# Performance work log

Hardware: AMD Instinct MI355X
Metric: run time of the kernel (lower is better)

The kernel has to match this reference:

```python
import jax, jax.numpy as jnp
import numpy as np


def setup_inputs() -> dict:
    key = jax.random.key(0)
    k1, k2, k3 = jax.random.split(key, 3)
    Na, Nb, D, K = 1024, 1024, 512, 256
    a = jax.random.normal(k1, (Na, D), dtype=jnp.float32)
    b = jax.random.normal(k2, (Nb, D), dtype=jnp.float32)
    feats = jax.random.normal(k3, (K, D), dtype=jnp.float32)
    return {"a": a, "b": b, "feats": feats}


def reference(a, b, feats):
    # 'ignorematch' mode of the Difference module.
    # Project both sets onto the feature bank: [Na,K] and [Nb,K]
    a_fk = jnp.matmul(a, feats.T)          # [Na, K]
    b_fk = jnp.matmul(b, feats.T)          # [Nb, K]
    a_e = a_fk[:, None, :]                 # [Na, 1, K]
    b_e = b_fk[None, :, :]                 # [1, Nb, K]
    # features present in a (>0) but absent in b (<=0)
    mask = ((a_e > 0) & (b_e <= 0)).astype(a_fk.dtype)  # [Na, Nb, K]
    result = jnp.sum(a_e * mask, axis=2)   # [Na, Nb]
    return result
```

## Files before the change

kernel.cpp:

```cpp
#include <hip/hip_runtime.h>
#include <hip/hip_bf16.h>


typedef short bf16x8 __attribute__((ext_vector_type(8)));
typedef float f32x4  __attribute__((ext_vector_type(4)));

__device__ inline void split2s(float x, short& h, short& m) {
    __hip_bfloat16 hb = __float2bfloat16(x);
    float r1 = x - __bfloat162float(hb);
    __hip_bfloat16 mb = __float2bfloat16(r1);
    h = *(short*)&hb; m = *(short*)&mb;
}

__device__ inline void split3s(float x, short& h, short& m, short& l) {
    __hip_bfloat16 hb = __float2bfloat16(x);
    float r1 = x - __bfloat162float(hb);
    __hip_bfloat16 mb = __float2bfloat16(r1);
    float r2 = r1 - __bfloat162float(mb);
    __hip_bfloat16 lb = __float2bfloat16(r2);
    h = *(short*)&hb; m = *(short*)&mb; l = *(short*)&lb;
}

__device__ inline void grid_barrier(unsigned* cnt, unsigned* flag, int nblk) {
    __syncthreads();
    if (threadIdx.x == 0) {
        __threadfence();
        unsigned prev = __hip_atomic_fetch_add(cnt, 1u, __ATOMIC_RELAXED,
                                               __HIP_MEMORY_SCOPE_AGENT);
        if (prev == (unsigned)(nblk - 1)) {
            __hip_atomic_store(flag, 1u, __ATOMIC_RELAXED, __HIP_MEMORY_SCOPE_AGENT);
        } else {
            while (__hip_atomic_load(flag, __ATOMIC_RELAXED,
                                     __HIP_MEMORY_SCOPE_AGENT) == 0u)
                __builtin_amdgcn_s_sleep(32);
        }
        __threadfence();
    }
    __syncthreads();
}

__global__ __launch_bounds__(256) void fused_kernel(
    const float* __restrict__ a, const float* __restrict__ b, const float* __restrict__ f,
    unsigned* __restrict__ bar,
    __hip_bfloat16* __restrict__ pbf, __hip_bfloat16* __restrict__ mbf,
    float* __restrict__ out)
{
    const int tid  = threadIdx.x;
    const int w    = tid >> 6;
    const int lane = tid & 63;
    const int l15  = lane & 15;
    const int q    = lane >> 4;

    {
        const int jb = blockIdx.x;
        const int m0 = (jb >> 3) * 32;
        const int n0 = (jb & 7) * 32;
        const int wi = w >> 1, wj = w & 1;

        const float* ap = a + (size_t)(m0 + wi * 16 + l15) * 512;
        const float* bp = b + (size_t)(m0 + wi * 16 + l15) * 512;
        const float* fp = f + (size_t)(n0 + wj * 16 + l15) * 512;

        f32x4 accA = {0.f, 0.f, 0.f, 0.f};
        f32x4 accB = {0.f, 0.f, 0.f, 0.f};

        #pragma unroll 2
        for (int k0 = 0; k0 < 512; k0 += 32) {
            const int ko = k0 + q * 8;
            float4 a0 = *(const float4*)(ap + ko);
            float4 a1 = *(const float4*)(ap + ko + 4);
            float4 b0 = *(const float4*)(bp + ko);
            float4 b1 = *(const float4*)(bp + ko + 4);
            float4 f0 = *(const float4*)(fp + ko);
            float4 f1 = *(const float4*)(fp + ko + 4);

            bf16x8 ah, am, bh, bm, bl, fh, fm, fl;
            const float av_[8] = {a0.x, a0.y, a0.z, a0.w, a1.x, a1.y, a1.z, a1.w};
            const float bv_[8] = {b0.x, b0.y, b0.z, b0.w, b1.x, b1.y, b1.z, b1.w};
            const float fv_[8] = {f0.x, f0.y, f0.z, f0.w, f1.x, f1.y, f1.z, f1.w};
            #pragma unroll
            for (int i = 0; i < 8; i++) {
                short h, m, l;
                split2s(av_[i], h, m);        ah[i] = h; am[i] = m;
                split3s(bv_[i], h, m, l);     bh[i] = h; bm[i] = m; bl[i] = l;
                split3s(fv_[i], h, m, l);     fh[i] = h; fm[i] = m; fl[i] = l;
            }

            accA = __builtin_amdgcn_mfma_f32_16x16x32_bf16(ah, fh, accA, 0, 0, 0);
            accB = __builtin_amdgcn_mfma_f32_16x16x32_bf16(bh, fh, accB, 0, 0, 0);
            accA = __builtin_amdgcn_mfma_f32_16x16x32_bf16(ah, fm, accA, 0, 0, 0);
            accB = __builtin_amdgcn_mfma_f32_16x16x32_bf16(bh, fm, accB, 0, 0, 0);
            accA = __builtin_amdgcn_mfma_f32_16x16x32_bf16(am, fh, accA, 0, 0, 0);
            accB = __builtin_amdgcn_mfma_f32_16x16x32_bf16(bm, fh, accB, 0, 0, 0);
            accB = __builtin_amdgcn_mfma_f32_16x16x32_bf16(bh, fl, accB, 0, 0, 0);
            accB = __builtin_amdgcn_mfma_f32_16x16x32_bf16(bl, fh, accB, 0, 0, 0);
            accB = __builtin_amdgcn_mfma_f32_16x16x32_bf16(bm, fm, accB, 0, 0, 0);
        }

        const int orow = m0 + wi * 16 + q * 4;
        const int ocol = n0 + wj * 16 + l15;
        #pragma unroll
        for (int r = 0; r < 4; r++) {
            pbf[(size_t)(orow + r) * 256 + ocol] = __float2bfloat16(fmaxf(accA[r], 0.f));
            mbf[(size_t)(orow + r) * 256 + ocol] = __float2bfloat16(accB[r] <= 0.f ? 1.f : 0.f);
        }
    }

    grid_barrier(bar + 0, bar + 16, gridDim.x);

    {
        const int i0 = (blockIdx.x >> 4) * 64;
        const int j0 = (blockIdx.x & 15) * 64;

        const short* ps = (const short*)pbf + (size_t)(i0 + w * 16 + l15) * 256;
        const short* ms = (const short*)mbf;

        f32x4 acc[4];
        #pragma unroll
        for (int c = 0; c < 4; c++) acc[c] = (f32x4){0.f, 0.f, 0.f, 0.f};

        #pragma unroll
        for (int k0 = 0; k0 < 256; k0 += 32) {
            const int ko = k0 + q * 8;
            bf16x8 av = *(const bf16x8*)(ps + ko);
            #pragma unroll
            for (int c = 0; c < 4; c++) {
                bf16x8 bv = *(const bf16x8*)(ms + (size_t)(j0 + c * 16 + l15) * 256 + ko);
                acc[c] = __builtin_amdgcn_mfma_f32_16x16x32_bf16(av, bv, acc[c], 0, 0, 0);
            }
        }

        const int orow = i0 + w * 16 + q * 4;
        const int ocol = j0 + l15;
        #pragma unroll
        for (int c = 0; c < 4; c++)
            #pragma unroll
            for (int r = 0; r < 4; r++)
                out[(size_t)(orow + r) * 1024 + ocol + c * 16] = acc[c][r];
    }
}

extern "C" void kernel_launch(void* const* d_in, const int* in_sizes, int n_in,
                              void* d_out, int out_size, void* d_ws, size_t ws_size,
                              hipStream_t stream) {
    const float* a     = (const float*)d_in[0];
    const float* b     = (const float*)d_in[1];
    const float* feats = (const float*)d_in[2];
    float* out = (float*)d_out;

    char* base = (char*)d_ws;
    unsigned* bar = (unsigned*)base;
    __hip_bfloat16* pbf = (__hip_bfloat16*)(base + 1024);
    __hip_bfloat16* mbf = pbf + 1024 * 256;

    hipMemsetAsync(bar, 0, 128, stream);
    fused_kernel<<<256, 256, 0, stream>>>(a, b, feats, bar, pbf, mbf, out);
}
```

Baseline: 91.78 us.

## Split fused grid-barrier kernel into two launches with finer work partition

```diff
diff --git a/kernel.cpp b/kernel.cpp
--- a/kernel.cpp
+++ b/kernel.cpp
@@ -5,138 +5,135 @@
 typedef short bf16x8 __attribute__((ext_vector_type(8)));
 typedef float f32x4  __attribute__((ext_vector_type(4)));
 
-__device__ inline void split2s(float x, short& h, short& m) {
-    __hip_bfloat16 hb = __float2bfloat16(x);
-    float r1 = x - __bfloat162float(hb);
-    __hip_bfloat16 mb = __float2bfloat16(r1);
-    h = *(short*)&hb; m = *(short*)&mb;
+__device__ inline void tsplit2_8(const float* x, bf16x8& h, bf16x8& m) {
+    #pragma unroll
+    for (int i = 0; i < 8; i++) {
+        unsigned xu = __float_as_uint(x[i]);
+        unsigned hu = xu & 0xFFFF0000u;
+        float r1 = x[i] - __uint_as_float(hu);
+        h[i] = (short)(xu >> 16);
+        m[i] = (short)(__float_as_uint(r1) >> 16);
+    }
 }
 
-__device__ inline void split3s(float x, short& h, short& m, short& l) {
-    __hip_bfloat16 hb = __float2bfloat16(x);
-    float r1 = x - __bfloat162float(hb);
-    __hip_bfloat16 mb = __float2bfloat16(r1);
-    float r2 = r1 - __bfloat162float(mb);
-    __hip_bfloat16 lb = __float2bfloat16(r2);
-    h = *(short*)&hb; m = *(short*)&mb; l = *(short*)&lb;
+__device__ inline void tsplit3_8(const float* x, bf16x8& h, bf16x8& m, bf16x8& l) {
+    #pragma unroll
+    for (int i = 0; i < 8; i++) {
+        unsigned xu = __float_as_uint(x[i]);
+        unsigned hu = xu & 0xFFFF0000u;
+        float r1 = x[i] - __uint_as_float(hu);
+        unsigned mu = __float_as_uint(r1) & 0xFFFF0000u;
+        float r2 = r1 - __uint_as_float(mu);
+        h[i] = (short)(xu >> 16);
+        m[i] = (short)(mu >> 16);
+        l[i] = (short)(__float_as_uint(r2) >> 16);
+    }
 }
 
-__device__ inline void grid_barrier(unsigned* cnt, unsigned* flag, int nblk) {
-    __syncthreads();
-    if (threadIdx.x == 0) {
-        __threadfence();
-        unsigned prev = __hip_atomic_fetch_add(cnt, 1u, __ATOMIC_RELAXED,
-                                               __HIP_MEMORY_SCOPE_AGENT);
-        if (prev == (unsigned)(nblk - 1)) {
-            __hip_atomic_store(flag, 1u, __ATOMIC_RELAXED, __HIP_MEMORY_SCOPE_AGENT);
-        } else {
-            while (__hip_atomic_load(flag, __ATOMIC_RELAXED,
-                                     __HIP_MEMORY_SCOPE_AGENT) == 0u)
-                __builtin_amdgcn_s_sleep(32);
-        }
-        __threadfence();
-    }
-    __syncthreads();
-}
-
-__global__ __launch_bounds__(256) void fused_kernel(
-    const float* __restrict__ a, const float* __restrict__ b, const float* __restrict__ f,
-    unsigned* __restrict__ bar,
-    __hip_bfloat16* __restrict__ pbf, __hip_bfloat16* __restrict__ mbf,
-    float* __restrict__ out)
+__global__ __launch_bounds__(256) void stage1_kernel(
+    const float* __restrict__ a, const float* __restrict__ b,
+    const float* __restrict__ f,
+    __hip_bfloat16* __restrict__ pbf, __hip_bfloat16* __restrict__ mbf)
 {
+    const int rt = blockIdx.x >> 3;
+    const int n0 = (blockIdx.x & 7) * 32;
     const int tid  = threadIdx.x;
     const int w    = tid >> 6;
     const int lane = tid & 63;
     const int l15  = lane & 15;
     const int q    = lane >> 4;
 
-    {
-        const int jb = blockIdx.x;
-        const int m0 = (jb >> 3) * 32;
-        const int n0 = (jb & 7) * 32;
-        const int wi = w >> 1, wj = w & 1;
+    const int r0 = rt * 16;
+    const int nw = n0 + (w & 1) * 16;
+    const bool isA = (w < 2);
 
-        const float* ap = a + (size_t)(m0 + wi * 16 + l15) * 512;
-        const float* bp = b + (size_t)(m0 + wi * 16 + l15) * 512;
-        const float* fp = f + (size_t)(n0 + wj * 16 + l15) * 512;
+    const float* xp = (isA ? a : b) + (size_t)(r0 + l15) * 512;
+    const float* fp = f + (size_t)(nw + l15) * 512;
 
-        f32x4 accA = {0.f, 0.f, 0.f, 0.f};
-        f32x4 accB = {0.f, 0.f, 0.f, 0.f};
+    f32x4 acc = {0.f, 0.f, 0.f, 0.f};
 
+    if (isA) {
         #pragma unroll 2
         for (int k0 = 0; k0 < 512; k0 += 32) {
             const int ko = k0 + q * 8;
-            float4 a0 = *(const float4*)(ap + ko);
-            float4 a1 = *(const float4*)(ap + ko + 4);
-            float4 b0 = *(const float4*)(bp + ko);
-            float4 b1 = *(const float4*)(bp + ko + 4);
-            float4 f0 = *(const float4*)(fp + ko);
-            float4 f1 = *(const float4*)(fp + ko + 4);
+            float xv[8], fv[8];
+            *(float4*)(xv)     = *(const float4*)(xp + ko);
+            *(float4*)(xv + 4) = *(const float4*)(xp + ko + 4);
+            *(float4*)(fv)     = *(const float4*)(fp + ko);
+            *(float4*)(fv + 4) = *(const float4*)(fp + ko + 4);
+            bf16x8 xh, xm, fh, fm;
+            tsplit2_8(xv, xh, xm);
+            tsplit2_8(fv, fh, fm);
+            acc = __builtin_amdgcn_mfma_f32_16x16x32_bf16(xh, fh, acc, 0, 0, 0);
+            acc = __builtin_amdgcn_mfma_f32_16x16x32_bf16(xh, fm, acc, 0, 0, 0);
+            acc = __builtin_amdgcn_mfma_f32_16x16x32_bf16(xm, fh, acc, 0, 0, 0);
+        }
+        #pragma unroll
+        for (int r = 0; r < 4; r++)
+            pbf[(size_t)(r0 + q * 4 + r) * 256 + nw + l15] =
+                __float2bfloat16(fmaxf(acc[r], 0.f));
+    } else {
+        #pragma unroll 2
+        for (int k0 = 0; k0 < 512; k0 += 32) {
+            const int ko = k0 + q * 8;
+            float xv[8], fv[8];
+            *(float4*)(xv)     = *(const float4*)(xp + ko);
+            *(float4*)(xv + 4) = *(const float4*)(xp + ko + 4);
+            *(float4*)(fv)     = *(const float4*)(fp + ko);
+            *(float4*)(fv + 4) = *(const float4*)(fp + ko + 4);
+            bf16x8 xh, xm, xl, fh, fm, fl;
+            tsplit3_8(xv, xh, xm, xl);
+            tsplit3_8(fv, fh, fm, fl);
+            acc = __builtin_amdgcn_mfma_f32_16x16x32_bf16(xh, fh, acc, 0, 0, 0);
+            acc = __builtin_amdgcn_mfma_f32_16x16x32_bf16(xh, fm, acc, 0, 0, 0);
+            acc = __builtin_amdgcn_mfma_f32_16x16x32_bf16(xm, fh, acc, 0, 0, 0);
+            acc = __builtin_amdgcn_mfma_f32_16x16x32_bf16(xh, fl, acc, 0, 0, 0);
+            acc = __builtin_amdgcn_mfma_f32_16x16x32_bf16(xl, fh, acc, 0, 0, 0);
+            acc = __builtin_amdgcn_mfma_f32_16x16x32_bf16(xm, fm, acc, 0, 0, 0);
+        }
+        #pragma unroll
+        for (int r = 0; r < 4; r++)
+            mbf[(size_t)(r0 + q * 4 + r) * 256 + nw + l15] =
+                __float2bfloat16(acc[r] <= 0.f ? 1.f : 0.f);
+    }
+}
 
-            bf16x8 ah, am, bh, bm, bl, fh, fm, fl;
-            const float av_[8] = {a0.x, a0.y, a0.z, a0.w, a1.x, a1.y, a1.z, a1.w};
-            const float bv_[8] = {b0.x, b0.y, b0.z, b0.w, b1.x, b1.y, b1.z, b1.w};
-            const float fv_[8] = {f0.x, f0.y, f0.z, f0.w, f1.x, f1.y, f1.z, f1.w};
-            #pragma unroll
-            for (int i = 0; i < 8; i++) {
-                short h, m, l;
-                split2s(av_[i], h, m);        ah[i] = h; am[i] = m;
-                split3s(bv_[i], h, m, l);     bh[i] = h; bm[i] = m; bl[i] = l;
-                split3s(fv_[i], h, m, l);     fh[i] = h; fm[i] = m; fl[i] = l;
-            }
+__global__ __launch_bounds__(256) void gemm2_kernel(
+    const __hip_bfloat16* __restrict__ p, const __hip_bfloat16* __restrict__ m,
+    float* __restrict__ out)
+{
+    const int i0 = (blockIdx.x >> 4) * 32;
+    const int j0 = (blockIdx.x & 15) * 64;
+    const int tid  = threadIdx.x;
+    const int w    = tid >> 6;
+    const int lane = tid & 63;
+    const int l15  = lane & 15;
+    const int q    = lane >> 4;
+    const int wi = w >> 1, wj = w & 1;
 
-            accA = __builtin_amdgcn_mfma_f32_16x16x32_bf16(ah, fh, accA, 0, 0, 0);
-            accB = __builtin_amdgcn_mfma_f32_16x16x32_bf16(bh, fh, accB, 0, 0, 0);
-            accA = __builtin_amdgcn_mfma_f32_16x16x32_bf16(ah, fm, accA, 0, 0, 0);
-            accB = __builtin_amdgcn_mfma_f32_16x16x32_bf16(bh, fm, accB, 0, 0, 0);
-            accA = __builtin_amdgcn_mfma_f32_16x16x32_bf16(am, fh, accA, 0, 0, 0);
-            accB = __builtin_amdgcn_mfma_f32_16x16x32_bf16(bm, fh, accB, 0, 0, 0);
-            accB = __builtin_amdgcn_mfma_f32_16x16x32_bf16(bh, fl, accB, 0, 0, 0);
-            accB = __builtin_amdgcn_mfma_f32_16x16x32_bf16(bl, fh, accB, 0, 0, 0);
-            accB = __builtin_amdgcn_mfma_f32_16x16x32_bf16(bm, fm, accB, 0, 0, 0);
-        }
+    const short* ps = (const short*)p + (size_t)(i0 + wi * 16 + l15) * 256;
+    const short* ms0 = (const short*)m + (size_t)(j0 + wj * 32 + l15) * 256;
+    const short* ms1 = ms0 + (size_t)16 * 256;
 
-        const int orow = m0 + wi * 16 + q * 4;
-        const int ocol = n0 + wj * 16 + l15;
-        #pragma unroll
-        for (int r = 0; r < 4; r++) {
-            pbf[(size_t)(orow + r) * 256 + ocol] = __float2bfloat16(fmaxf(accA[r], 0.f));
-            mbf[(size_t)(orow + r) * 256 + ocol] = __float2bfloat16(accB[r] <= 0.f ? 1.f : 0.f);
-        }
+    f32x4 acc0 = {0.f, 0.f, 0.f, 0.f};
+    f32x4 acc1 = {0.f, 0.f, 0.f, 0.f};
+
+    #pragma unroll
+    for (int k0 = 0; k0 < 256; k0 += 32) {
+        const int ko = k0 + q * 8;
+        bf16x8 av = *(const bf16x8*)(ps  + ko);
+        bf16x8 b0 = *(const bf16x8*)(ms0 + ko);
+        bf16x8 b1 = *(const bf16x8*)(ms1 + ko);
+        acc0 = __builtin_amdgcn_mfma_f32_16x16x32_bf16(av, b0, acc0, 0, 0, 0);
+        acc1 = __builtin_amdgcn_mfma_f32_16x16x32_bf16(av, b1, acc1, 0, 0, 0);
     }
 
-    grid_barrier(bar + 0, bar + 16, gridDim.x);
-
-    {
-        const int i0 = (blockIdx.x >> 4) * 64;
-        const int j0 = (blockIdx.x & 15) * 64;
-
-        const short* ps = (const short*)pbf + (size_t)(i0 + w * 16 + l15) * 256;
-        const short* ms = (const short*)mbf;
-
-        f32x4 acc[4];
-        #pragma unroll
-        for (int c = 0; c < 4; c++) acc[c] = (f32x4){0.f, 0.f, 0.f, 0.f};
-
-        #pragma unroll
-        for (int k0 = 0; k0 < 256; k0 += 32) {
-            const int ko = k0 + q * 8;
-            bf16x8 av = *(const bf16x8*)(ps + ko);
-            #pragma unroll
-            for (int c = 0; c < 4; c++) {
-                bf16x8 bv = *(const bf16x8*)(ms + (size_t)(j0 + c * 16 + l15) * 256 + ko);
-                acc[c] = __builtin_amdgcn_mfma_f32_16x16x32_bf16(av, bv, acc[c], 0, 0, 0);
-            }
-        }
-
-        const int orow = i0 + w * 16 + q * 4;
-        const int ocol = j0 + l15;
-        #pragma unroll
-        for (int c = 0; c < 4; c++)
-            #pragma unroll
-            for (int r = 0; r < 4; r++)
-                out[(size_t)(orow + r) * 1024 + ocol + c * 16] = acc[c][r];
+    const int orow = i0 + wi * 16 + q * 4;
+    const int ocol = j0 + wj * 32 + l15;
+    #pragma unroll
+    for (int r = 0; r < 4; r++) {
+        out[(size_t)(orow + r) * 1024 + ocol]      = acc0[r];
+        out[(size_t)(orow + r) * 1024 + ocol + 16] = acc1[r];
     }
 }
 
@@ -148,11 +145,9 @@
     const float* feats = (const float*)d_in[2];
     float* out = (float*)d_out;
 
-    char* base = (char*)d_ws;
-    unsigned* bar = (unsigned*)base;
-    __hip_bfloat16* pbf = (__hip_bfloat16*)(base + 1024);
+    __hip_bfloat16* pbf = (__hip_bfloat16*)d_ws;
     __hip_bfloat16* mbf = pbf + 1024 * 256;
 
-    hipMemsetAsync(bar, 0, 128, stream);
-    fused_kernel<<<256, 256, 0, stream>>>(a, b, feats, bar, pbf, mbf, out);
+    stage1_kernel<<<512, 256, 0, stream>>>(a, b, feats, pbf, mbf);
+    gemm2_kernel <<<512, 256, 0, stream>>>(pbf, mbf, out);
 }
```

Measured after the change: 83.32 us. 9.2% less time.
